# Optimization experiments

Hardware: AMD Instinct MI355X
Metric: run time of the kernel (lower is better)

## Reference

```python
import jax, jax.numpy as jnp
import numpy as np

L_SIDE = 32
N_PIX = 12 * L_SIDE * L_SIDE      # 12288 sphere pixels
N_VALID = N_PIX // 2              # theta <= pi/2 hemisphere (first half by construction)
A_TH, B_TH, C_TH = 0.03, 1.0, 1.0  # ellipsoid semi-axes (thickness, 1, 1)


def _sphere_angles(n):
    # Deterministic Fibonacci-lattice sphere sampling standing in for SphereHealpix.
    i = np.arange(n, dtype=np.float64)
    z = 1.0 - 2.0 * (i + 0.5) / n          # cos(theta), descending -> theta<=pi/2 iff i < n/2
    theta = np.arccos(z)
    phi = (i * np.pi * (3.0 - np.sqrt(5.0))) % (2.0 * np.pi)
    return theta.astype(np.float32), phi.astype(np.float32)


def _ellipse_valid():
    # Faithful translation of ReconstructionModel.ellipse_valid for the valid hemisphere.
    theta_all, phi_all = _sphere_angles(N_PIX)
    tv = theta_all[:N_VALID].astype(np.float32)
    pv = phi_all[:N_VALID].astype(np.float32)
    a, b, c = np.float32(A_TH), np.float32(B_TH), np.float32(C_TH)
    # cartesian coords of valid pixels (computed BEFORE the angle shift)
    xv = np.cos(pv) * np.sin(tv)
    yv = np.sin(pv) * np.sin(tv)
    # meshgrid(phi, x) / meshgrid(theta, y) with ij indexing -> angles vary on rows, coords on cols
    phi = ((pv + np.pi / 2) % (2 * np.pi)).astype(np.float32)[:, None]   # [Nv,1]
    theta = ((tv + np.pi / 2) % np.pi).astype(np.float32)[:, None]       # [Nv,1]
    x = xv[None, :]
    y = yv[None, :]
    x_c = np.sin(2 * theta) / 2 * np.cos(phi)
    y_c = -np.sin(2 * theta) / 2 * np.sin(phi)
    z_c = (np.cos(2 * theta) + 1) / 2
    r = np.sqrt(2 * (np.cos(2 * theta) + 1)) / 2 + np.float32(1e-5)
    a2, b2, c2 = a * a, b * b, c * c
    ct, st = np.cos(theta), np.sin(theta)
    cp, sp = np.cos(phi), np.sin(phi)
    ct2, ct4 = ct ** 2, ct ** 4
    cp2 = cp ** 2
    x2, y2 = x ** 2, y ** 2
    s2p = np.sin(2.0 * phi)
    with np.errstate(invalid='ignore'):
        S = (-b2 * ct2 + b2 * ct4 - b2 * y2 - c2 * x2
             + a2 * b2 * ct4 + b2 * c2 * ct2 - b2 * c2 * ct4
             - b2 * x2 * cp2 + b2 * y2 * cp2 + c2 * x2 * cp2 - c2 * y2 * cp2
             - a2 * x2 * ct2 + c2 * x2 * ct2
             + b2 * x * y * s2p - c2 * x * y * s2p
             + a2 * x2 * cp2 * ct2 - a2 * y2 * cp2 * ct2
             - c2 * x2 * cp2 * ct2 + c2 * y2 * cp2 * ct2
             + 2.0 * b2 * x * cp * ct * st - 2.0 * b2 * y * ct * sp * st
             + 2.0 * c2 * x * y * cp * ct2 * sp - 2.0 * a2 * x * y * cp * ct2 * sp)
        num = (a * c * np.sqrt(S)
               - a2 * b * ct2 + 2.0 * a2 * b * ct4
               + 2.0 * b * c2 * ct2 - 2.0 * b * c2 * ct4
               + a2 * b * x * cp * ct * st - b * c2 * x * cp * ct * st
               - a2 * b * y * ct * sp * st + b * c2 * y * ct * sp * st)
        den = b * (a2 * ct2 - c2 * ct2 + c2)
        z = num / den
        f = ((x - x_c) ** 2 + (y - y_c) ** 2 + (z - z_c) ** 2) / r ** 2
    f = np.where(np.isnan(f), np.float32(0.0), f)   # f[f != f] = 0
    return f.astype(np.float32)


def setup_inputs() -> dict:
    key = jax.random.key(0)
    x = jax.random.uniform(key, (8, 16, N_PIX), dtype=jnp.float32)
    all_responses = jnp.asarray(_ellipse_valid())   # [N_VALID, N_VALID]
    return {"x": x, "all_responses": all_responses}


def reference(x, all_responses):
    nv = all_responses.shape[0]
    # masked gather: theta <= pi/2 is exactly the first nv pixels by construction
    x_valid = x[:, :, :nv]                                   # [B,C,Nv]
    mixture = jnp.einsum('bcn,nm->bcm', x_valid, all_responses)
    mixture = jnp.clip(mixture, 0.0, 1.0)                    # mix='clip'
    # masked scatter back into zero buffer
    out = jnp.zeros_like(x).at[:, :, :nv].set(mixture)
    return out
```

## Files before the change

kernel.cpp:

```cpp
#include <hip/hip_runtime.h>
#include <hip/hip_bf16.h>


#define NPIX 12288
#define NV   6144
#define MR   128
#define KST  128
#define LDA  6208
#define LDP  6208
#define PARTF ((size_t)MR * LDP)

typedef __attribute__((ext_vector_type(8))) short bf16x8;
typedef __attribute__((ext_vector_type(4))) float f32x4;
typedef __attribute__((ext_vector_type(4))) unsigned u32x4;

__device__ __forceinline__ unsigned pk2(float lo, float hi) {
    __hip_bfloat162 h = __float22bfloat162_rn(make_float2(lo, hi));
    union { __hip_bfloat162 h; unsigned u; } v; v.h = h; return v.u;
}

__global__ __launch_bounds__(256) void prep_kernel(const float* __restrict__ x,
                                                   unsigned short* __restrict__ abf) {
    int q = blockIdx.x * 256 + threadIdx.x;
    int m = q / (NV / 8);
    int r = q % (NV / 8);
    int k = r * 8;
    const float* src = x + (size_t)m * NPIX + k;
    f32x4 a = *(const f32x4*)(src);
    f32x4 b = *(const f32x4*)(src + 4);
    u32x4 o;
    o[0] = pk2(a[0], a[1]); o[1] = pk2(a[2], a[3]);
    o[2] = pk2(b[0], b[1]); o[3] = pk2(b[2], b[3]);
    *(u32x4*)(abf + (size_t)m * LDA + k) = o;
}

__device__ __forceinline__ void sload3(const float*& rp, f32x4 (&r)[8]) {
    #pragma unroll
    for (int j = 0; j < 8; ++j) r[j] = *(const f32x4*)(rp + (size_t)j * NV);
    rp += (size_t)KST * NV;
}

__device__ __forceinline__ void wstage3(unsigned char* buf, const f32x4 (&r)[8],
                                        int q, int kb) {
    #pragma unroll
    for (int c = 0; c < 4; ++c) {
        const int n_loc = q * 4 + c;
        u32x4 o;
        o[0] = pk2(r[0][c], r[1][c]);
        o[1] = pk2(r[2][c], r[3][c]);
        o[2] = pk2(r[4][c], r[5][c]);
        o[3] = pk2(r[6][c], r[7][c]);
        *(u32x4*)(buf + n_loc * 256 + (kb ^ ((n_loc & 7) << 4))) = o;
    }
}

__device__ __forceinline__ void compute3(const unsigned char* buf,
        const unsigned short* __restrict__ A,
        size_t arow0, size_t arow1, int ln, int lg, f32x4 (&acc)[2][4]) {
    bf16x8 afr[2][4];
    #pragma unroll
    for (int ks = 0; ks < 4; ++ks) {
        afr[0][ks] = *(const bf16x8*)(A + arow0 + ks * 32);
        afr[1][ks] = *(const bf16x8*)(A + arow1 + ks * 32);
    }
    const int swn = (ln & 7) << 4;
    #pragma unroll
    for (int nt = 0; nt < 4; ++nt) {
        const int rowb = (nt * 16 + ln) * 256;
        #pragma unroll
        for (int ks = 0; ks < 4; ++ks) {
            bf16x8 bfr = *(const bf16x8*)(buf + rowb + (((lg * 16) + ks * 64) ^ swn));
            acc[0][nt] = __builtin_amdgcn_mfma_f32_16x16x32_bf16(afr[0][ks], bfr, acc[0][nt], 0, 0, 0);
            acc[1][nt] = __builtin_amdgcn_mfma_f32_16x16x32_bf16(afr[1][ks], bfr, acc[1][nt], 0, 0, 0);
        }
    }
}

__global__ __launch_bounds__(256) void gemm3_kernel(
        const unsigned short* __restrict__ A,
        const float* __restrict__ R,
        float* __restrict__ wpart) {
    __shared__ __align__(64) unsigned char Bs0[16384];
    __shared__ __align__(64) unsigned char Bs1[16384];

    const int tid = threadIdx.x;
    const int w = tid >> 6, l = tid & 63;
    const int ln = l & 15, lg = l >> 4;
    const int q = ln;
    const int chunk = blockIdx.x & 7;
    const int nb = blockIdx.x >> 3;
    const int n0 = nb * 64;
    const int kbase = chunk * 768;
    const int nsi = 768 / KST;
    const int kb = w * 64 + lg * 16;

    const float* rp = R + (size_t)(kbase + w * 32 + lg * 8) * NV + n0 + q * 4;

    size_t arow0 = (size_t)(w * 32 + ln) * LDA + kbase + lg * 8;
    size_t arow1 = arow0 + (size_t)16 * LDA;

    f32x4 acc[2][4];
    #pragma unroll
    for (int a = 0; a < 2; ++a)
        #pragma unroll
        for (int b = 0; b < 4; ++b) {
            acc[a][b][0] = 0.f; acc[a][b][1] = 0.f;
            acc[a][b][2] = 0.f; acc[a][b][3] = 0.f;
        }

    f32x4 ring0[8], ring1[8];
    sload3(rp, ring0);
    sload3(rp, ring1);
    wstage3(Bs0, ring0, q, kb);
    __syncthreads();

    #pragma unroll 1
    for (int it = 0; it < nsi / 2; ++it) {
        const int s = it * 2;
        if (s + 2 < nsi) sload3(rp, ring0);
        compute3(Bs0, A, arow0, arow1, ln, lg, acc);
        arow0 += KST; arow1 += KST;
        wstage3(Bs1, ring1, q, kb);
        __syncthreads();
        if (s + 3 < nsi) sload3(rp, ring1);
        compute3(Bs1, A, arow0, arow1, ln, lg, acc);
        arow0 += KST; arow1 += KST;
        if (s + 2 < nsi) wstage3(Bs0, ring0, q, kb);
        __syncthreads();
    }

    float* dst = wpart + (size_t)chunk * PARTF;
    #pragma unroll
    for (int mt = 0; mt < 2; ++mt) {
        const int mbase = w * 32 + mt * 16 + lg * 4;
        #pragma unroll
        for (int nt = 0; nt < 4; ++nt) {
            const size_t cb = (size_t)(n0 + nt * 16 + ln);
            #pragma unroll
            for (int j = 0; j < 4; ++j)
                dst[(size_t)(mbase + j) * LDP + cb] = acc[mt][nt][j];
        }
    }
}

__global__ __launch_bounds__(256) void reduce_kernel(float* __restrict__ out,
        const float* __restrict__ wpart) {
    int q = blockIdx.x * 256 + threadIdx.x;
    int m = q / (NV / 4);
    int r = q % (NV / 4);
    f32x4 a;
    a[0] = 0.f; a[1] = 0.f; a[2] = 0.f; a[3] = 0.f;
    #pragma unroll 1
    for (int p = 0; p < 8; ++p) {
        f32x4 c = *(const f32x4*)(wpart + (size_t)p * PARTF + (size_t)m * LDP + r * 4);
        #pragma unroll
        for (int i = 0; i < 4; ++i) a[i] += c[i];
    }
    f32x4 cz, z;
    #pragma unroll
    for (int i = 0; i < 4; ++i) {
        cz[i] = fminf(fmaxf(a[i], 0.f), 1.f);
        z[i] = 0.f;
    }
    size_t base = (size_t)m * NPIX + r * 4;
    *(f32x4*)(out + base) = cz;
    *(f32x4*)(out + base + NV) = z;
}

typedef float2 fl2;
__device__ __forceinline__ bf16x8 cvt8(f32x4 a, f32x4 b) {
    union { unsigned u[4]; bf16x8 v; } r;
    r.u[0] = pk2(a[0], a[1]); r.u[1] = pk2(a[2], a[3]);
    r.u[2] = pk2(b[0], b[1]); r.u[3] = pk2(b[2], b[3]);
    return r.v;
}
__device__ __forceinline__ void sload(const float*& bptr, fl2 (&r)[8]) {
    #pragma unroll
    for (int gi = 0; gi < 4; ++gi) {
        const float* p = bptr + (size_t)(gi * 32) * NV;
        r[2 * gi]     = *(const fl2*)(p);
        r[2 * gi + 1] = *(const fl2*)(p + NV);
    }
    bptr += (size_t)KST * NV;
}
__device__ __forceinline__ void wstage(unsigned char* buf, const fl2 (&r)[8],
                                       int kq, int nq, int sw0, int sw1) {
    #pragma unroll
    for (int gi = 0; gi < 4; ++gi) {
        unsigned lo = pk2(r[2 * gi].x, r[2 * gi + 1].x);
        unsigned hi = pk2(r[2 * gi].y, r[2 * gi + 1].y);
        const int kbyte = (kq + gi * 32) * 2;
        *(unsigned*)(buf + nq * 256       + (kbyte ^ sw0)) = lo;
        *(unsigned*)(buf + (nq + 1) * 256 + (kbyte ^ sw1)) = hi;
    }
}
__device__ __forceinline__ void compute_fb(const unsigned char* buf,
        const float* __restrict__ X, size_t arow0, size_t arow1,
        int ln, int lg, f32x4 (&acc)[2][2]) {
    bf16x8 afr[2][4];
    #pragma unroll
    for (int ks = 0; ks < 4; ++ks) {
        f32x4 p0 = *(const f32x4*)(X + arow0 + ks * 32);
        f32x4 p1 = *(const f32x4*)(X + arow0 + ks * 32 + 4);
        afr[0][ks] = cvt8(p0, p1);
        f32x4 q0 = *(const f32x4*)(X + arow1 + ks * 32);
        f32x4 q1 = *(const f32x4*)(X + arow1 + ks * 32 + 4);
        afr[1][ks] = cvt8(q0, q1);
    }
    const int swn = (ln & 7) << 4;
    #pragma unroll
    for (int nt = 0; nt < 2; ++nt) {
        const int rowb = (nt * 16 + ln) * 256;
        #pragma unroll
        for (int ks = 0; ks < 4; ++ks) {
            bf16x8 bfr = *(const bf16x8*)(buf + rowb + (((lg * 16) + ks * 64) ^ swn));
            acc[0][nt] = __builtin_amdgcn_mfma_f32_16x16x32_bf16(afr[0][ks], bfr, acc[0][nt], 0, 0, 0);
            acc[1][nt] = __builtin_amdgcn_mfma_f32_16x16x32_bf16(afr[1][ks], bfr, acc[1][nt], 0, 0, 0);
        }
    }
}
__global__ __launch_bounds__(256) void gemm_fb_kernel(const float* __restrict__ X,
        const float* __restrict__ R, float* __restrict__ out) {
    __shared__ unsigned char Bs0[32 * 256];
    __shared__ unsigned char Bs1[32 * 256];
    const int tid = threadIdx.x;
    const int w = tid >> 6, l = tid & 63;
    const int ln = l & 15, lg = l >> 4;
    const int chunk = blockIdx.x / 192;
    const int nb = blockIdx.x % 192;
    const int n0 = nb * 32;
    const int kbase = chunk * (NV / 2);
    const int nsi = (NV / 2) / KST;
    const int kq = (tid >> 4) * 2;
    const int nq = (tid & 15) * 2;
    const float* bptr = R + (size_t)(kbase + kq) * NV + (n0 + nq);
    const int sw0 = (nq & 7) << 4;
    const int sw1 = ((nq + 1) & 7) << 4;
    size_t arow0 = (size_t)(w * 32 + ln) * NPIX + kbase + lg * 8;
    size_t arow1 = arow0 + (size_t)16 * NPIX;
    f32x4 acc[2][2];
    #pragma unroll
    for (int a = 0; a < 2; ++a)
        #pragma unroll
        for (int b = 0; b < 2; ++b) {
            acc[a][b][0] = 0.f; acc[a][b][1] = 0.f;
            acc[a][b][2] = 0.f; acc[a][b][3] = 0.f;
        }
    fl2 ring0[8], ring1[8];
    sload(bptr, ring0);
    sload(bptr, ring1);
    wstage(Bs0, ring0, kq, nq, sw0, sw1);
    __syncthreads();
    #pragma unroll 1
    for (int it = 0; it < nsi / 2; ++it) {
        const int s = it * 2;
        if (s + 2 < nsi) sload(bptr, ring0);
        compute_fb(Bs0, X, arow0, arow1, ln, lg, acc);
        arow0 += KST; arow1 += KST;
        wstage(Bs1, ring1, kq, nq, sw0, sw1);
        __syncthreads();
        if (s + 3 < nsi) sload(bptr, ring1);
        compute_fb(Bs1, X, arow0, arow1, ln, lg, acc);
        arow0 += KST; arow1 += KST;
        if (s + 2 < nsi) wstage(Bs0, ring0, kq, nq, sw0, sw1);
        __syncthreads();
    }
    float* dst = out + (size_t)chunk * NV;
    #pragma unroll
    for (int mt = 0; mt < 2; ++mt) {
        const int mbase = w * 32 + mt * 16 + lg * 4;
        #pragma unroll
        for (int nt = 0; nt < 2; ++nt) {
            const size_t cb = (size_t)(n0 + nt * 16 + ln);
            #pragma unroll
            for (int j = 0; j < 4; ++j)
                dst[(size_t)(mbase + j) * NPIX + cb] = acc[mt][nt][j];
        }
    }
}
__global__ __launch_bounds__(256) void reduce_fb_kernel(float* __restrict__ out) {
    int q = blockIdx.x * 256 + threadIdx.x;
    int m = q / (NV / 4);
    int r = q % (NV / 4);
    size_t base = (size_t)m * NPIX + r * 4;
    f32x4 a = *(f32x4*)(out + base);
    f32x4 b = *(f32x4*)(out + base + NV);
    f32x4 cz, z;
    #pragma unroll
    for (int i = 0; i < 4; ++i) {
        float v = a[i] + b[i];
        cz[i] = fminf(fmaxf(v, 0.f), 1.f);
        z[i] = 0.f;
    }
    *(f32x4*)(out + base) = cz;
    *(f32x4*)(out + base + NV) = z;
}

extern "C" void kernel_launch(void* const* d_in, const int* in_sizes, int n_in,
                              void* d_out, int out_size, void* d_ws, size_t ws_size,
                              hipStream_t stream) {
    const float* x = (const float*)d_in[0];
    const float* R = (const float*)d_in[1];
    float* out = (float*)d_out;

    const size_t abytes = (size_t)MR * LDA * 2;
    const size_t wbytes = 8 * PARTF * 4;

    if (ws_size >= abytes + wbytes) {
        unsigned short* abf = (unsigned short*)d_ws;
        float* wpart = (float*)((char*)d_ws + abytes);
        prep_kernel<<<(MR * NV / 8) / 256, 256, 0, stream>>>(x, abf);
        gemm3_kernel<<<96 * 8, 256, 0, stream>>>(abf, R, wpart);
        reduce_kernel<<<(MR * NV / 4) / 256, 256, 0, stream>>>(out, wpart);
    } else {
        gemm_fb_kernel<<<192 * 2, 256, 0, stream>>>(x, R, out);
        reduce_fb_kernel<<<(MR * NV / 4) / 256, 256, 0, stream>>>(out);
    }
}
```

Baseline: 236.3 us.

## Restructure split-K GEMM with larger 128x256 tiles, 16 K-chunks, fragment-layout partials

```diff
diff --git a/kernel.cpp b/kernel.cpp
--- a/kernel.cpp
+++ b/kernel.cpp
@@ -5,10 +5,14 @@
 #define NPIX 12288
 #define NV   6144
 #define MR   128
-#define KST  128
 #define LDA  6208
-#define LDP  6208
-#define PARTF ((size_t)MR * LDP)
+#define CH   16
+#define KCH  384
+#define KST4 64
+#define BN4  256
+#define NSI4 6
+#define REGF 4096
+#define SLOTF ((size_t)192 * REGF)
 
 typedef __attribute__((ext_vector_type(8))) short bf16x8;
 typedef __attribute__((ext_vector_type(4))) float f32x4;
@@ -17,6 +21,10 @@
 __device__ __forceinline__ unsigned pk2(float lo, float hi) {
     __hip_bfloat162 h = __float22bfloat162_rn(make_float2(lo, hi));
     union { __hip_bfloat162 h; unsigned u; } v; v.h = h; return v.u;
+}
+
+__device__ __forceinline__ int swz(int row) {
+    return ((row ^ (row >> 3)) & 7) << 4;
 }
 
 __global__ __launch_bounds__(256) void prep_kernel(const float* __restrict__ x,
@@ -34,74 +42,71 @@
     *(u32x4*)(abf + (size_t)m * LDA + k) = o;
 }
 
-__device__ __forceinline__ void sload3(const float*& rp, f32x4 (&r)[8]) {
+__device__ __forceinline__ void sload4(const float*& rp, f32x4 (&r)[8]) {
     #pragma unroll
     for (int j = 0; j < 8; ++j) r[j] = *(const f32x4*)(rp + (size_t)j * NV);
-    rp += (size_t)KST * NV;
-}
-
-__device__ __forceinline__ void wstage3(unsigned char* buf, const f32x4 (&r)[8],
-                                        int q, int kb) {
+    rp += (size_t)KST4 * NV;
+}
+
+__device__ __forceinline__ void wstage4(unsigned char* buf, const f32x4 (&r)[8],
+                                        int l, int w) {
     #pragma unroll
     for (int c = 0; c < 4; ++c) {
-        const int n_loc = q * 4 + c;
+        const int row = l * 4 + c;
         u32x4 o;
         o[0] = pk2(r[0][c], r[1][c]);
         o[1] = pk2(r[2][c], r[3][c]);
         o[2] = pk2(r[4][c], r[5][c]);
         o[3] = pk2(r[6][c], r[7][c]);
-        *(u32x4*)(buf + n_loc * 256 + (kb ^ ((n_loc & 7) << 4))) = o;
-    }
-}
-
-__device__ __forceinline__ void compute3(const unsigned char* buf,
-        const unsigned short* __restrict__ A,
-        size_t arow0, size_t arow1, int ln, int lg, f32x4 (&acc)[2][4]) {
-    bf16x8 afr[2][4];
-    #pragma unroll
-    for (int ks = 0; ks < 4; ++ks) {
-        afr[0][ks] = *(const bf16x8*)(A + arow0 + ks * 32);
-        afr[1][ks] = *(const bf16x8*)(A + arow1 + ks * 32);
-    }
-    const int swn = (ln & 7) << 4;
+        *(u32x4*)(buf + row * 128 + ((w * 16) ^ swz(row))) = o;
+    }
+}
+
+__device__ __forceinline__ void compute4(const unsigned char* buf,
+        const unsigned short* __restrict__ A, size_t abase,
+        int wn, int ln, int lg, f32x4 (&acc)[4][4]) {
+    bf16x8 afr[4][2];
+    #pragma unroll
+    for (int mt = 0; mt < 4; ++mt)
+        #pragma unroll
+        for (int ks = 0; ks < 2; ++ks)
+            afr[mt][ks] = *(const bf16x8*)(A + abase + (size_t)(mt * 16) * LDA + ks * 32);
     #pragma unroll
     for (int nt = 0; nt < 4; ++nt) {
-        const int rowb = (nt * 16 + ln) * 256;
-        #pragma unroll
-        for (int ks = 0; ks < 4; ++ks) {
-            bf16x8 bfr = *(const bf16x8*)(buf + rowb + (((lg * 16) + ks * 64) ^ swn));
-            acc[0][nt] = __builtin_amdgcn_mfma_f32_16x16x32_bf16(afr[0][ks], bfr, acc[0][nt], 0, 0, 0);
-            acc[1][nt] = __builtin_amdgcn_mfma_f32_16x16x32_bf16(afr[1][ks], bfr, acc[1][nt], 0, 0, 0);
-        }
-    }
-}
-
-__global__ __launch_bounds__(256) void gemm3_kernel(
+        const int row = wn * 64 + nt * 16 + ln;
+        const int sw = swz(row);
+        #pragma unroll
+        for (int ks = 0; ks < 2; ++ks) {
+            bf16x8 bfr = *(const bf16x8*)(buf + row * 128 + (((ks * 4 + lg) * 16) ^ sw));
+            #pragma unroll
+            for (int mt = 0; mt < 4; ++mt)
+                acc[mt][nt] = __builtin_amdgcn_mfma_f32_16x16x32_bf16(afr[mt][ks], bfr, acc[mt][nt], 0, 0, 0);
+        }
+    }
+}
+
+__global__ __launch_bounds__(512) void gemm4_kernel(
         const unsigned short* __restrict__ A,
         const float* __restrict__ R,
-        float* __restrict__ wpart) {
-    __shared__ __align__(64) unsigned char Bs0[16384];
-    __shared__ __align__(64) unsigned char Bs1[16384];
+        float* __restrict__ part) {
+    __shared__ __align__(16) unsigned char Bs0[BN4 * 128];
+    __shared__ __align__(16) unsigned char Bs1[BN4 * 128];
 
     const int tid = threadIdx.x;
     const int w = tid >> 6, l = tid & 63;
-    const int ln = l & 15, lg = l >> 4;
-    const int q = ln;
-    const int chunk = blockIdx.x & 7;
-    const int nb = blockIdx.x >> 3;
-    const int n0 = nb * 64;
-    const int kbase = chunk * 768;
-    const int nsi = 768 / KST;
-    const int kb = w * 64 + lg * 16;
-
-    const float* rp = R + (size_t)(kbase + w * 32 + lg * 8) * NV + n0 + q * 4;
-
-    size_t arow0 = (size_t)(w * 32 + ln) * LDA + kbase + lg * 8;
-    size_t arow1 = arow0 + (size_t)16 * LDA;
-
-    f32x4 acc[2][4];
-    #pragma unroll
-    for (int a = 0; a < 2; ++a)
+    const int ln = l & 15, lg = (l >> 4) & 3;
+    const int wm = w >> 2, wn = w & 3;
+    const int chunk = blockIdx.x & 15;
+    const int nb = blockIdx.x >> 4;
+    const int n0 = nb * BN4;
+    const int kbase = chunk * KCH;
+
+    const float* rp = R + (size_t)(kbase + w * 8) * NV + n0 + l * 4;
+    const size_t abase = (size_t)(wm * 64 + ln) * LDA + kbase + lg * 8;
+
+    f32x4 acc[4][4];
+    #pragma unroll
+    for (int a = 0; a < 4; ++a)
         #pragma unroll
         for (int b = 0; b < 4; ++b) {
             acc[a][b][0] = 0.f; acc[a][b][1] = 0.f;
@@ -109,62 +114,70 @@
         }
 
     f32x4 ring0[8], ring1[8];
-    sload3(rp, ring0);
-    sload3(rp, ring1);
-    wstage3(Bs0, ring0, q, kb);
+    sload4(rp, ring0);
+    sload4(rp, ring1);
+    wstage4(Bs0, ring0, l, w);
     __syncthreads();
 
     #pragma unroll 1
-    for (int it = 0; it < nsi / 2; ++it) {
+    for (int it = 0; it < NSI4 / 2; ++it) {
         const int s = it * 2;
-        if (s + 2 < nsi) sload3(rp, ring0);
-        compute3(Bs0, A, arow0, arow1, ln, lg, acc);
-        arow0 += KST; arow1 += KST;
-        wstage3(Bs1, ring1, q, kb);
+        if (s + 2 < NSI4) sload4(rp, ring0);
+        compute4(Bs0, A, abase + (size_t)s * KST4, wn, ln, lg, acc);
+        wstage4(Bs1, ring1, l, w);
         __syncthreads();
-        if (s + 3 < nsi) sload3(rp, ring1);
-        compute3(Bs1, A, arow0, arow1, ln, lg, acc);
-        arow0 += KST; arow1 += KST;
-        if (s + 2 < nsi) wstage3(Bs0, ring0, q, kb);
+        if (s + 3 < NSI4) sload4(rp, ring1);
+        compute4(Bs1, A, abase + (size_t)(s + 1) * KST4, wn, ln, lg, acc);
+        if (s + 2 < NSI4) wstage4(Bs0, ring0, l, w);
         __syncthreads();
     }
 
-    float* dst = wpart + (size_t)chunk * PARTF;
-    #pragma unroll
-    for (int mt = 0; mt < 2; ++mt) {
-        const int mbase = w * 32 + mt * 16 + lg * 4;
-        #pragma unroll
-        for (int nt = 0; nt < 4; ++nt) {
-            const size_t cb = (size_t)(n0 + nt * 16 + ln);
+    float* dst = part + ((((size_t)chunk * 24 + nb) * 8 + w) << 12);
+    #pragma unroll
+    for (int mt = 0; mt < 4; ++mt)
+        #pragma unroll
+        for (int nt = 0; nt < 4; ++nt)
+            *(f32x4*)(dst + ((((mt * 4 + nt) << 6) + l) << 2)) = acc[mt][nt];
+}
+
+__global__ __launch_bounds__(256) void reduce4_kernel(float* __restrict__ out,
+        const float* __restrict__ part) {
+    __shared__ float T[64][68];
+    const int t = threadIdx.x;
+    const int nb = blockIdx.x >> 3, w = blockIdx.x & 7;
+    const int lg = (t >> 4) & 3, ln = t & 15, hi = t >> 6;
+    const size_t rbase = (((size_t)nb * 8 + w) << 12);
+
+    #pragma unroll 1
+    for (int u = 0; u < 4; ++u) {
+        const size_t off = rbase + u * 1024 + t * 4;
+        f32x4 s;
+        s[0] = 0.f; s[1] = 0.f; s[2] = 0.f; s[3] = 0.f;
+        #pragma unroll
+        for (int c = 0; c < CH; ++c) {
+            const f32x4 v = *(const f32x4*)(part + (size_t)c * SLOTF + off);
             #pragma unroll
-            for (int j = 0; j < 4; ++j)
-                dst[(size_t)(mbase + j) * LDP + cb] = acc[mt][nt][j];
-        }
-    }
-}
-
-__global__ __launch_bounds__(256) void reduce_kernel(float* __restrict__ out,
-        const float* __restrict__ wpart) {
-    int q = blockIdx.x * 256 + threadIdx.x;
-    int m = q / (NV / 4);
-    int r = q % (NV / 4);
-    f32x4 a;
-    a[0] = 0.f; a[1] = 0.f; a[2] = 0.f; a[3] = 0.f;
-    #pragma unroll 1
-    for (int p = 0; p < 8; ++p) {
-        f32x4 c = *(const f32x4*)(wpart + (size_t)p * PARTF + (size_t)m * LDP + r * 4);
-        #pragma unroll
-        for (int i = 0; i < 4; ++i) a[i] += c[i];
-    }
-    f32x4 cz, z;
-    #pragma unroll
-    for (int i = 0; i < 4; ++i) {
-        cz[i] = fminf(fmaxf(a[i], 0.f), 1.f);
-        z[i] = 0.f;
-    }
-    size_t base = (size_t)m * NPIX + r * 4;
-    *(f32x4*)(out + base) = cz;
-    *(f32x4*)(out + base + NV) = z;
+            for (int i = 0; i < 4; ++i) s[i] += v[i];
+        }
+        const int nloc = hi * 16 + ln;
+        #pragma unroll
+        for (int j = 0; j < 4; ++j)
+            T[u * 16 + lg * 4 + j][nloc] = fminf(fmaxf(s[j], 0.f), 1.f);
+    }
+    __syncthreads();
+
+    const int r = t >> 2, sq = t & 3;
+    const size_t orow = (size_t)((w >> 2) * 64 + r) * NPIX
+                      + (size_t)nb * 256 + (w & 3) * 64;
+    #pragma unroll
+    for (int u = 0; u < 4; ++u) {
+        const int col = u * 16 + sq * 4;
+        f32x4 v = *(const f32x4*)(&T[r][col]);
+        *(f32x4*)(out + orow + col) = v;
+        f32x4 z;
+        z[0] = 0.f; z[1] = 0.f; z[2] = 0.f; z[3] = 0.f;
+        *(f32x4*)(out + orow + NV + col) = z;
+    }
 }
 
 typedef float2 fl2;
@@ -181,7 +194,7 @@
         r[2 * gi]     = *(const fl2*)(p);
         r[2 * gi + 1] = *(const fl2*)(p + NV);
     }
-    bptr += (size_t)KST * NV;
+    bptr += (size_t)128 * NV;
 }
 __device__ __forceinline__ void wstage(unsigned char* buf, const fl2 (&r)[8],
                                        int kq, int nq, int sw0, int sw1) {
@@ -230,7 +243,7 @@
     const int nb = blockIdx.x % 192;
     const int n0 = nb * 32;
     const int kbase = chunk * (NV / 2);
-    const int nsi = (NV / 2) / KST;
+    const int nsi = (NV / 2) / 128;
     const int kq = (tid >> 4) * 2;
     const int nq = (tid & 15) * 2;
     const float* bptr = R + (size_t)(kbase + kq) * NV + (n0 + nq);
@@ -256,12 +269,12 @@
         const int s = it * 2;
         if (s + 2 < nsi) sload(bptr, ring0);
         compute_fb(Bs0, X, arow0, arow1, ln, lg, acc);
-        arow0 += KST; arow1 += KST;
+        arow0 += 128; arow1 += 128;
         wstage(Bs1, ring1, kq, nq, sw0, sw1);
         __syncthreads();
         if (s + 3 < nsi) sload(bptr, ring1);
         compute_fb(Bs1, X, arow0, arow1, ln, lg, acc);
-        arow0 += KST; arow1 += KST;
+        arow0 += 128; arow1 += 128;
         if (s + 2 < nsi) wstage(Bs0, ring0, kq, nq, sw0, sw1);
         __syncthreads();
     }
@@ -304,14 +317,14 @@
     float* out = (float*)d_out;
 
     const size_t abytes = (size_t)MR * LDA * 2;
-    const size_t wbytes = 8 * PARTF * 4;
-
-    if (ws_size >= abytes + wbytes) {
+    const size_t pbytes = (size_t)CH * SLOTF * 4;
+
+    if (ws_size >= abytes + pbytes) {
         unsigned short* abf = (unsigned short*)d_ws;
-        float* wpart = (float*)((char*)d_ws + abytes);
+        float* part = (float*)((char*)d_ws + abytes);
         prep_kernel<<<(MR * NV / 8) / 256, 256, 0, stream>>>(x, abf);
-        gemm3_kernel<<<96 * 8, 256, 0, stream>>>(abf, R, wpart);
-        reduce_kernel<<<(MR * NV / 4) / 256, 256, 0, stream>>>(out, wpart);
+        gemm4_kernel<<<24 * CH, 512, 0, stream>>>(abf, R, part);
+        reduce4_kernel<<<24 * 8, 256, 0, stream>>>(out, part);
     } else {
         gemm_fb_kernel<<<192 * 2, 256, 0, stream>>>(x, R, out);
         reduce_fb_kernel<<<(MR * NV / 4) / 256, 256, 0, stream>>>(out);
```

Result: slower. 249.9 us (+5.7%).
